# Performance work log

Hardware: AMD Instinct MI355X
Metric: run time of the kernel (lower is better)

The kernel has to match this reference:

```python
import jax, jax.numpy as jnp
import numpy as np

BIGINT = 1e10

def sinusoidal_embed(pos, dim):
    # SinusoidalPositionEmbedding: interleaved sin/cos, matches torch reshape order
    idx = jnp.arange(dim // 2, dtype=jnp.float32)
    freq = jnp.power(10000.0, -2.0 * idx / dim)
    ang = pos.astype(jnp.float32)[:, None] * freq[None, :]          # [N, d/2]
    emb = jnp.stack([jnp.sin(ang), jnp.cos(ang)], axis=-1)          # [N, d/2, 2]
    return emb.reshape(pos.shape[0], dim)

def dihedral(a, b, c, d):
    # standard signed dihedral angle of four points, [...,3] -> [...]
    u1, u2, u3 = b - a, c - b, d - c
    n1 = jnp.cross(u1, u2)
    n2 = jnp.cross(u2, u3)
    u2n = u2 / (jnp.linalg.norm(u2, axis=-1, keepdims=True) + 1e-12)
    m = jnp.cross(n1, u2n)
    x = jnp.sum(n1 * n2, axis=-1)
    y = jnp.sum(m * n2, axis=-1)
    return jnp.arctan2(y, x)

def knn_edges(X, Seg, bid, k):
    # faithful dense formulation of _construct_knn: pairwise min-over-channel-pair
    # distance, masked by (same bid) & (same Seg), then smallest-k per row.
    N = X.shape[0]
    rule = (bid[:, None] == bid[None, :]) & (Seg[:, None] == Seg[None, :])  # [N,N]
    sq = jnp.sum(X * X, axis=-1)                                   # [N,C]
    dot = jnp.einsum('icd,jed->icje', X, X)                        # [N,C,N,C]
    d2 = sq[:, :, None, None] + sq[None, None, :, :] - 2.0 * dot   # [N,C,N,C]
    dmin = jnp.sqrt(jnp.maximum(jnp.min(d2, axis=(1, 3)), 0.0))    # [N,N]
    dist = jnp.where(rule, dmin, BIGINT)
    neg_vals, dst = jax.lax.top_k(-dist, k)                        # smallest-k
    dnb = -neg_vals                                                # [N,k]
    src = jnp.broadcast_to(jnp.arange(N)[:, None], (N, k))
    valid = (dnb < BIGINT).reshape(-1)                             # [N*k]
    dst = dst.reshape(-1)
    src = src.reshape(-1)
    # torch compacts invalid edges (dynamic shape); we pad them with -1 + mask
    edges = jnp.stack([jnp.where(valid, dst, -1), jnp.where(valid, src, -1)])
    return edges, valid

def pairwise_dihedrals(X, dst, src):
    # inter-residue dihedrals on backbone atoms, channels = [N, CA, C, O]
    ir_phi = dihedral(X[dst, 2], X[src, 0], X[src, 1], X[src, 2])  # C_i, N_j, CA_j, C_j
    ir_psi = dihedral(X[dst, 0], X[dst, 1], X[dst, 2], X[src, 0])  # N_i, CA_i, C_i, N_j
    return jnp.stack([ir_phi, ir_psi], axis=-1)                    # [E, 2]

def setup_inputs() -> dict:
    key = jax.random.key(0)
    ks = jax.random.split(key, 8)
    N, C, E, NUM_AA, NUM_ID = 3000, 4, 64, 21, 2
    X = jax.random.normal(ks[0], (N, C, 3), dtype=jnp.float32) * 10.0
    S = jax.random.randint(ks[1], (N,), 0, NUM_AA)
    RP = jax.random.randint(ks[2], (N,), 0, 1000)
    ID = jax.random.randint(ks[3], (N,), 0, NUM_ID)
    Seg = jax.random.randint(ks[4], (N,), 0, 2)
    bid = jnp.sort(jax.random.randint(ks[5], (N,), 0, 8))
    res_embed = jax.random.normal(ks[6], (NUM_AA, E), dtype=jnp.float32)
    id_embed = jax.random.normal(ks[7], (NUM_ID, E), dtype=jnp.float32)
    return {"X": X, "S": S, "RP": RP, "ID": ID, "Seg": Seg, "bid": bid,
            "res_embed": res_embed, "id_embed": id_embed, "k_neighbors": 10}

def reference(X, S, RP, ID, Seg, bid, res_embed, id_embed, k_neighbors):
    # node features: [residue embedding, positional + chain-id embedding]
    res_h = res_embed[S]                                           # [N,E]
    rp_h = sinusoidal_embed(RP, res_embed.shape[1]) + id_embed[ID] # [N,E]
    H = jnp.concatenate([res_h, rp_h], axis=-1)                    # [N,2E]
    edges, valid = knn_edges(X, Seg, bid, k_neighbors)             # [2,N*k], [N*k]
    dst = jnp.maximum(edges[0], 0)
    src = jnp.maximum(edges[1], 0)
    edge_attr = pairwise_dihedrals(X, dst, src)                    # [N*k,2]
    edge_attr = jnp.where(valid[:, None], edge_attr, 0.0)
    return H, edges, edge_attr, valid
```

## Files before the change

kernel.cpp:

```cpp
#include <hip/hip_runtime.h>
#include <math.h>

#define TOPK 10
#define WAVE 64
#define NGROUPS 16
#define MAXC 256
#define MAXM 4

__device__ __forceinline__ void cross3(const float* a, const float* b, float* o) {
    o[0] = a[1] * b[2] - a[2] * b[1];
    o[1] = a[2] * b[0] - a[0] * b[2];
    o[2] = a[0] * b[1] - a[1] * b[0];
}
__device__ __forceinline__ float dot3(const float* a, const float* b) {
    return a[0] * b[0] + a[1] * b[1] + a[2] * b[2];
}

__device__ float dihedral4(const float* a, const float* b, const float* c, const float* d) {
    float u1[3], u2[3], u3[3];
    #pragma unroll
    for (int t = 0; t < 3; t++) {
        u1[t] = b[t] - a[t];
        u2[t] = c[t] - b[t];
        u3[t] = d[t] - c[t];
    }
    float n1[3], n2[3];
    cross3(u1, u2, n1);
    cross3(u2, u3, n2);
    float nrm = sqrtf(dot3(u2, u2)) + 1e-12f;
    float u2n[3] = {u2[0] / nrm, u2[1] / nrm, u2[2] / nrm};
    float m[3];
    cross3(n1, u2n, m);
    float x = dot3(n1, n2);
    float y = dot3(m, n2);
    return atan2f(y, x);
}

__device__ __forceinline__ void load_xrow(const float4* __restrict__ X4, int j,
                                          float xj[4][3]) {
    float4 a = X4[j * 3 + 0];
    float4 b = X4[j * 3 + 1];
    float4 c = X4[j * 3 + 2];
    xj[0][0] = a.x; xj[0][1] = a.y; xj[0][2] = a.z;
    xj[1][0] = a.w; xj[1][1] = b.x; xj[1][2] = b.y;
    xj[2][0] = b.z; xj[2][1] = b.w; xj[2][2] = c.x;
    xj[3][0] = c.y; xj[3][1] = c.z; xj[3][2] = c.w;
}

__global__ void node_feat_groups_kernel(
    const float* __restrict__ res_embed,
    const float* __restrict__ id_embed,
    const int* __restrict__ S,
    const int* __restrict__ RP,
    const int* __restrict__ ID,
    const int* __restrict__ Seg,
    const int* __restrict__ bid,
    float* __restrict__ H,
    int* __restrict__ lists,
    int* __restrict__ counts,
    int N, int E) {
    int idx = blockIdx.x * blockDim.x + threadIdx.x;
    int lane = threadIdx.x & (WAVE - 1);

    if (idx < N) {
        int g = (bid[idx] << 1) | Seg[idx];
        #pragma unroll
        for (int G = 0; G < NGROUPS; G++) {
            bool mine = (g == G);
            unsigned long long m = __ballot(mine);
            if (m) {
                int leader = (int)(__ffsll((long long)m) - 1);
                int base = 0;
                if (lane == leader) base = atomicAdd(&counts[G], (int)__popcll(m));
                base = __shfl(base, leader, WAVE);
                if (mine) {
                    int pos = base + (int)__popcll(m & ((1ull << lane) - 1ull));
                    lists[(size_t)G * N + pos] = idx;
                }
            }
        }
    }

    if (idx < N * E) {
        int n = idx / E;
        int e = idx - n * E;
        float* Hrow = H + (size_t)n * 2 * E;
        Hrow[e] = res_embed[S[n] * E + e];
        if (e < E / 2) {
            int half = e;
            float freq = exp2f((float)half * (-2.0f * 13.287712379549449f / 64.0f));
            float ang = (float)RP[n] * freq;
            float s, c;
            __sincosf(ang, &s, &c);
            const float* idrow = id_embed + ID[n] * E;
            Hrow[E + 2 * half + 0] = s + idrow[2 * half + 0];
            Hrow[E + 2 * half + 1] = c + idrow[2 * half + 1];
        }
    }
}

__global__ __launch_bounds__(WAVE) void knn_rows_kernel(
    const float* __restrict__ X,
    const int* __restrict__ Seg,
    const int* __restrict__ bid,
    const int* __restrict__ lists,
    const int* __restrict__ counts,
    float* __restrict__ out_e0,
    float* __restrict__ out_e1,
    float* __restrict__ out_attr,
    float* __restrict__ out_valid,
    int N) {
    __shared__ unsigned long long keys[MAXC];

    const int i = blockIdx.x;
    const int lane = threadIdx.x;
    const float4* X4 = (const float4*)X;

    float xi[4][3], sqi[4];
    load_xrow(X4, i, xi);
    #pragma unroll
    for (int c = 0; c < 4; c++)
        sqi[c] = xi[c][0] * xi[c][0] + xi[c][1] * xi[c][1] + xi[c][2] * xi[c][2];

    const int g = (bid[i] << 1) | Seg[i];
    int cnt = counts[g];
    if (cnt > MAXC) cnt = MAXC;
    const int* list = lists + (size_t)g * N;
    const int mmax = (cnt + WAVE - 1) >> 6;

    const unsigned long long EMPTY = ~0ull;
    unsigned long long own[MAXM];
    #pragma unroll
    for (int m = 0; m < MAXM; m++) own[m] = EMPTY;

    for (int m = 0; m < mmax; m++) {
        int t = m * WAVE + lane;
        if (t < cnt) {
            int j = list[t];
            float xj[4][3], sqj[4];
            load_xrow(X4, j, xj);
            #pragma unroll
            for (int c = 0; c < 4; c++)
                sqj[c] = xj[c][0] * xj[c][0] + xj[c][1] * xj[c][1] + xj[c][2] * xj[c][2];

            float bestd2 = 3.4e38f;
            #pragma unroll
            for (int c = 0; c < 4; c++) {
                #pragma unroll
                for (int e = 0; e < 4; e++) {
                    float dp = xi[c][0] * xj[e][0] + xi[c][1] * xj[e][1] +
                               xi[c][2] * xj[e][2];
                    float d2 = (sqi[c] + sqj[e]) - 2.0f * dp;
                    bestd2 = fminf(bestd2, d2);
                }
            }
            float dist = sqrtf(fmaxf(bestd2, 0.0f));
            unsigned long long key =
                ((unsigned long long)__float_as_uint(dist) << 32) | (unsigned)j;
            own[m] = key;
            keys[t] = key;
        }
    }
    __syncthreads();

    int rank[MAXM];
    #pragma unroll
    for (int m = 0; m < MAXM; m++) rank[m] = 0;

    const ulonglong2* k2 = (const ulonglong2*)keys;
    const int quads = cnt >> 2;
    for (int q = 0; q < quads; q++) {
        ulonglong2 ka = k2[2 * q + 0];
        ulonglong2 kb = k2[2 * q + 1];
        #pragma unroll
        for (int m = 0; m < MAXM; m++) {
            rank[m] += (ka.x < own[m]) ? 1 : 0;
            rank[m] += (ka.y < own[m]) ? 1 : 0;
            rank[m] += (kb.x < own[m]) ? 1 : 0;
            rank[m] += (kb.y < own[m]) ? 1 : 0;
        }
    }
    for (int r = quads << 2; r < cnt; r++) {
        unsigned long long kr = keys[r];
        #pragma unroll
        for (int m = 0; m < MAXM; m++) rank[m] += (kr < own[m]) ? 1 : 0;
    }

    if (cnt < TOPK && lane >= cnt && lane < TOPK) {
        int e = i * TOPK + lane;
        out_e0[e] = -1.0f;
        out_e1[e] = -1.0f;
        out_valid[e] = 0.0f;
        out_attr[e * 2 + 0] = 0.0f;
        out_attr[e * 2 + 1] = 0.0f;
    }
    for (int m = 0; m < mmax; m++) {
        if (own[m] != EMPTY && rank[m] < TOPK) {
            int j = (int)(own[m] & 0xffffffffu);
            int e = i * TOPK + rank[m];
            out_e0[e] = (float)j;
            out_e1[e] = (float)i;
            out_valid[e] = 1.0f;
            float xj[4][3];
            load_xrow(X4, j, xj);
            float phi = dihedral4(xj[2], xi[0], xi[1], xi[2]);
            float psi = dihedral4(xj[0], xj[1], xj[2], xi[0]);
            out_attr[e * 2 + 0] = phi;
            out_attr[e * 2 + 1] = psi;
        }
    }
}

extern "C" void kernel_launch(void* const* d_in, const int* in_sizes, int n_in,
                              void* d_out, int out_size, void* d_ws, size_t ws_size,
                              hipStream_t stream) {
    const float* X = (const float*)d_in[0];
    const int* S = (const int*)d_in[1];
    const int* RP = (const int*)d_in[2];
    const int* ID = (const int*)d_in[3];
    const int* Seg = (const int*)d_in[4];
    const int* bid = (const int*)d_in[5];
    const float* res_embed = (const float*)d_in[6];
    const float* id_embed = (const float*)d_in[7];

    const int N = in_sizes[1];
    const int E = 64;

    float* out = (float*)d_out;
    float* H = out;
    float* e0 = H + (size_t)N * 2 * E;
    float* e1 = e0 + (size_t)N * TOPK;
    float* attr = e1 + (size_t)N * TOPK;
    float* validp = attr + (size_t)N * TOPK * 2;

    int* counts = (int*)d_ws;
    int* lists = (int*)((char*)d_ws + 256);

    hipMemsetAsync(counts, 0, NGROUPS * sizeof(int), stream);

    int total = N * E;
    hipLaunchKernelGGL(node_feat_groups_kernel, dim3((total + 255) / 256), dim3(256), 0,
                       stream, res_embed, id_embed, S, RP, ID, Seg, bid, H, lists, counts,
                       N, E);
    hipLaunchKernelGGL(knn_rows_kernel, dim3(N), dim3(WAVE), 0, stream,
                       X, Seg, bid, lists, counts, e0, e1, attr, validp, N);
}
```

Before: 95.47 us.

## Fuse node features and KNN into one kernel using sorted-bid range search

Drops the separate group-building kernel, its memset and the atomics. Each block now finds its batch range in the sorted bid array with a two-level ballot search, filters candidates by Seg inline, and compacts keys into shared memory with ballot and popcount. Node embedding is computed in the same block, and ranking is specialised by the number of candidate chunks. This removes two launches and a global intermediate list. In exchange every row repeats the binary search, and the candidate scan now covers the whole batch range, not only the same-Seg members.

Measured after the change: 92.18 us. -3.4%, faster.

```diff
diff --git a/kernel.cpp b/kernel.cpp
--- a/kernel.cpp
+++ b/kernel.cpp
@@ -3,7 +3,6 @@
 
 #define TOPK 10
 #define WAVE 64
-#define NGROUPS 16
 #define MAXC 256
 #define MAXM 4
 
@@ -47,98 +46,118 @@
     xj[3][0] = c.y; xj[3][1] = c.z; xj[3][2] = c.w;
 }
 
-__global__ void node_feat_groups_kernel(
-    const float* __restrict__ res_embed,
-    const float* __restrict__ id_embed,
+template <int M>
+__device__ __forceinline__ void rank_all(const unsigned long long* __restrict__ keys,
+                                         int cnt, const unsigned long long own[MAXM],
+                                         int rank[MAXM]) {
+    const ulonglong2* k2 = (const ulonglong2*)keys;
+    const int quads = cnt >> 2;
+    for (int q = 0; q < quads; q++) {
+        ulonglong2 ka = k2[2 * q + 0];
+        ulonglong2 kb = k2[2 * q + 1];
+        #pragma unroll
+        for (int m = 0; m < M; m++) {
+            rank[m] += (ka.x < own[m]) ? 1 : 0;
+            rank[m] += (ka.y < own[m]) ? 1 : 0;
+            rank[m] += (kb.x < own[m]) ? 1 : 0;
+            rank[m] += (kb.y < own[m]) ? 1 : 0;
+        }
+    }
+    for (int r = quads << 2; r < cnt; r++) {
+        unsigned long long kr = keys[r];
+        #pragma unroll
+        for (int m = 0; m < M; m++) rank[m] += (kr < own[m]) ? 1 : 0;
+    }
+}
+
+__device__ __forceinline__ int find_first(const int* __restrict__ bid, int s, int e,
+                                          int b, bool strict, int dflt, int lane) {
+    int q = s + lane;
+    bool in = (q <= e);
+    int v = in ? bid[q] : 0;
+    bool pred = in && (strict ? (v > b) : (v >= b));
+    unsigned long long m = __ballot(pred);
+    if (m == 0ull) return dflt;
+    return s + (int)(__ffsll((long long)m) - 1);
+}
+
+__global__ __launch_bounds__(WAVE) void fused_graph_kernel(
+    const float* __restrict__ X,
     const int* __restrict__ S,
     const int* __restrict__ RP,
     const int* __restrict__ ID,
     const int* __restrict__ Seg,
     const int* __restrict__ bid,
+    const float* __restrict__ res_embed,
+    const float* __restrict__ id_embed,
     float* __restrict__ H,
-    int* __restrict__ lists,
-    int* __restrict__ counts,
-    int N, int E) {
-    int idx = blockIdx.x * blockDim.x + threadIdx.x;
-    int lane = threadIdx.x & (WAVE - 1);
-
-    if (idx < N) {
-        int g = (bid[idx] << 1) | Seg[idx];
-        #pragma unroll
-        for (int G = 0; G < NGROUPS; G++) {
-            bool mine = (g == G);
-            unsigned long long m = __ballot(mine);
-            if (m) {
-                int leader = (int)(__ffsll((long long)m) - 1);
-                int base = 0;
-                if (lane == leader) base = atomicAdd(&counts[G], (int)__popcll(m));
-                base = __shfl(base, leader, WAVE);
-                if (mine) {
-                    int pos = base + (int)__popcll(m & ((1ull << lane) - 1ull));
-                    lists[(size_t)G * N + pos] = idx;
-                }
-            }
-        }
-    }
-
-    if (idx < N * E) {
-        int n = idx / E;
-        int e = idx - n * E;
-        float* Hrow = H + (size_t)n * 2 * E;
-        Hrow[e] = res_embed[S[n] * E + e];
-        if (e < E / 2) {
-            int half = e;
-            float freq = exp2f((float)half * (-2.0f * 13.287712379549449f / 64.0f));
-            float ang = (float)RP[n] * freq;
-            float s, c;
-            __sincosf(ang, &s, &c);
-            const float* idrow = id_embed + ID[n] * E;
-            Hrow[E + 2 * half + 0] = s + idrow[2 * half + 0];
-            Hrow[E + 2 * half + 1] = c + idrow[2 * half + 1];
-        }
-    }
-}
-
-__global__ __launch_bounds__(WAVE) void knn_rows_kernel(
-    const float* __restrict__ X,
-    const int* __restrict__ Seg,
-    const int* __restrict__ bid,
-    const int* __restrict__ lists,
-    const int* __restrict__ counts,
     float* __restrict__ out_e0,
     float* __restrict__ out_e1,
     float* __restrict__ out_attr,
     float* __restrict__ out_valid,
-    int N) {
-    __shared__ unsigned long long keys[MAXC];
+    int N, int E) {
+    __shared__ __align__(16) unsigned long long keys[MAXC];
 
     const int i = blockIdx.x;
     const int lane = threadIdx.x;
     const float4* X4 = (const float4*)X;
 
+    {
+        float* Hrow = H + (size_t)i * 2 * E;
+        Hrow[lane] = res_embed[S[i] * E + lane];
+        if (lane < E / 2) {
+            int half = lane;
+            float freq = exp2f((float)half * (-2.0f * 13.287712379549449f / 64.0f));
+            float ang = (float)RP[i] * freq;
+            float s, c;
+            __sincosf(ang, &s, &c);
+            const float2 idv = *(const float2*)(id_embed + ID[i] * E + 2 * half);
+            float2 o;
+            o.x = s + idv.x;
+            o.y = c + idv.y;
+            *(float2*)(Hrow + E + 2 * half) = o;
+        }
+    }
+
     float xi[4][3], sqi[4];
     load_xrow(X4, i, xi);
     #pragma unroll
     for (int c = 0; c < 4; c++)
         sqi[c] = xi[c][0] * xi[c][0] + xi[c][1] * xi[c][1] + xi[c][2] * xi[c][2];
 
-    const int g = (bid[i] << 1) | Seg[i];
-    int cnt = counts[g];
-    if (cnt > MAXC) cnt = MAXC;
-    const int* list = lists + (size_t)g * N;
-    const int mmax = (cnt + WAVE - 1) >> 6;
+    const int b = bid[i];
+    const int segI = Seg[i];
+
+    int p = (lane * N) >> 6;
+    int vb = bid[p];
+    unsigned long long mge = __ballot(vb >= b);
+    unsigned long long mgt = __ballot(vb > b);
+    int lo, hi;
+    if (mge == 0ull) {
+        lo = find_first(bid, ((63 * N) >> 6) + 1, N - 1, b, false, N, lane);
+    } else {
+        int f = (int)(__ffsll((long long)mge) - 1);
+        lo = (f == 0) ? 0
+                      : find_first(bid, (((f - 1) * N) >> 6) + 1, (f * N) >> 6, b,
+                                   false, N, lane);
+    }
+    if (mgt == 0ull) {
+        hi = find_first(bid, ((63 * N) >> 6) + 1, N - 1, b, true, N, lane);
+    } else {
+        int f = (int)(__ffsll((long long)mgt) - 1);
+        hi = find_first(bid, (((f - 1) * N) >> 6) + 1, (f * N) >> 6, b, true, N, lane);
+    }
 
     const unsigned long long EMPTY = ~0ull;
-    unsigned long long own[MAXM];
-    #pragma unroll
-    for (int m = 0; m < MAXM; m++) own[m] = EMPTY;
-
-    for (int m = 0; m < mmax; m++) {
-        int t = m * WAVE + lane;
-        if (t < cnt) {
-            int j = list[t];
+    int cbase = 0;
+    for (int base = lo; base < hi; base += WAVE) {
+        int t = base + lane;
+        bool act = false;
+        unsigned long long key = EMPTY;
+        if (t < hi && Seg[t] == segI) {
+            act = true;
             float xj[4][3], sqj[4];
-            load_xrow(X4, j, xj);
+            load_xrow(X4, t, xj);
             #pragma unroll
             for (int c = 0; c < 4; c++)
                 sqj[c] = xj[c][0] * xj[c][0] + xj[c][1] * xj[c][1] + xj[c][2] * xj[c][2];
@@ -155,36 +174,37 @@
                 }
             }
             float dist = sqrtf(fmaxf(bestd2, 0.0f));
-            unsigned long long key =
-                ((unsigned long long)__float_as_uint(dist) << 32) | (unsigned)j;
-            own[m] = key;
-            keys[t] = key;
-        }
-    }
+            key = ((unsigned long long)__float_as_uint(dist) << 32) | (unsigned)t;
+        }
+        unsigned long long mask = __ballot(act);
+        int pos = cbase + (int)__popcll(mask & ((1ull << lane) - 1ull));
+        if (act && pos < MAXC) keys[pos] = key;
+        cbase += (int)__popcll(mask);
+    }
+    int cnt = (cbase < MAXC) ? cbase : MAXC;
+
     __syncthreads();
 
+    unsigned long long own[MAXM];
     int rank[MAXM];
     #pragma unroll
-    for (int m = 0; m < MAXM; m++) rank[m] = 0;
-
-    const ulonglong2* k2 = (const ulonglong2*)keys;
-    const int quads = cnt >> 2;
-    for (int q = 0; q < quads; q++) {
-        ulonglong2 ka = k2[2 * q + 0];
-        ulonglong2 kb = k2[2 * q + 1];
-        #pragma unroll
-        for (int m = 0; m < MAXM; m++) {
-            rank[m] += (ka.x < own[m]) ? 1 : 0;
-            rank[m] += (ka.y < own[m]) ? 1 : 0;
-            rank[m] += (kb.x < own[m]) ? 1 : 0;
-            rank[m] += (kb.y < own[m]) ? 1 : 0;
-        }
-    }
-    for (int r = quads << 2; r < cnt; r++) {
-        unsigned long long kr = keys[r];
-        #pragma unroll
-        for (int m = 0; m < MAXM; m++) rank[m] += (kr < own[m]) ? 1 : 0;
-    }
+    for (int m = 0; m < MAXM; m++) {
+        own[m] = EMPTY;
+        rank[m] = 0;
+    }
+    const int m2max = (cnt + WAVE - 1) >> 6;
+    #pragma unroll
+    for (int m = 0; m < MAXM; m++) {
+        int t = m * WAVE + lane;
+        if (m < m2max && t < cnt) own[m] = keys[t];
+    }
+
+    if (m2max <= 2)
+        rank_all<2>(keys, cnt, own, rank);
+    else if (m2max == 3)
+        rank_all<3>(keys, cnt, own, rank);
+    else
+        rank_all<4>(keys, cnt, own, rank);
 
     if (cnt < TOPK && lane >= cnt && lane < TOPK) {
         int e = i * TOPK + lane;
@@ -194,7 +214,8 @@
         out_attr[e * 2 + 0] = 0.0f;
         out_attr[e * 2 + 1] = 0.0f;
     }
-    for (int m = 0; m < mmax; m++) {
+    #pragma unroll
+    for (int m = 0; m < MAXM; m++) {
         if (own[m] != EMPTY && rank[m] < TOPK) {
             int j = (int)(own[m] & 0xffffffffu);
             int e = i * TOPK + rank[m];
@@ -233,15 +254,9 @@
     float* attr = e1 + (size_t)N * TOPK;
     float* validp = attr + (size_t)N * TOPK * 2;
 
-    int* counts = (int*)d_ws;
-    int* lists = (int*)((char*)d_ws + 256);
-
-    hipMemsetAsync(counts, 0, NGROUPS * sizeof(int), stream);
-
-    int total = N * E;
-    hipLaunchKernelGGL(node_feat_groups_kernel, dim3((total + 255) / 256), dim3(256), 0,
-                       stream, res_embed, id_embed, S, RP, ID, Seg, bid, H, lists, counts,
-                       N, E);
-    hipLaunchKernelGGL(knn_rows_kernel, dim3(N), dim3(WAVE), 0, stream,
-                       X, Seg, bid, lists, counts, e0, e1, attr, validp, N);
-}
+    (void)d_ws;
+    (void)ws_size;
+    hipLaunchKernelGGL(fused_graph_kernel, dim3(N), dim3(WAVE), 0, stream,
+                       X, S, RP, ID, Seg, bid, res_embed, id_embed,
+                       H, e0, e1, attr, validp, N, E);
+}
```
